# Performance work log

Hardware: AMD Instinct MI355X
Metric: run time of the kernel (lower is better)

The kernel has to match this reference:

```python
import jax, jax.numpy as jnp
import numpy as np


def setup_inputs() -> dict:
    key = jax.random.key(0)
    k1, k2 = jax.random.split(key)
    N, D = 8192, 64
    mag = jax.random.uniform(k1, (N, D), dtype=jnp.float32)
    phase = jax.random.normal(k2, (N, D), dtype=jnp.float32)
    return {"mag": mag, "phase": phase}


def reference(mag, phase):
    # score_ij = sum_d mag_i,d * mag_j,d * cos(phase_i,d - phase_j,d)
    # expanded via cos(a-b) = cos a cos b + sin a sin b into two GEMMs,
    # mathematically identical to the O(N^2 D) broadcasted form.
    a = mag * jnp.cos(phase)  # [N, D]
    b = mag * jnp.sin(phase)  # [N, D]
    scores = a @ a.T + b @ b.T  # [N, N]
    attn = jax.nn.softmax(scores, axis=1)
    new_mag = attn @ mag      # [N, D]
    new_phase = attn @ phase  # [N, D]
    return new_mag, new_phase
```

## Files before the change

kernel.cpp:

```cpp
#include <hip/hip_runtime.h>
#include <hip/hip_bf16.h>

typedef __attribute__((ext_vector_type(8))) short short8;
typedef __attribute__((ext_vector_type(4))) float f32x4;
typedef __attribute__((ext_vector_type(16))) float f32x16;
typedef __attribute__((ext_vector_type(2))) int int2v;

#define N_TOK 8192
#define D_HALF 64
#define D_FULL 128
#define QB 64
#define KHALF 4096
#define CHUNK 128
#define NCH (KHALF / CHUNK)
#define OSTR 132
#define THR 8.0f

__global__ __launch_bounds__(256) void precompute_kernel(
    const float* __restrict__ mag, const float* __restrict__ phase,
    __hip_bfloat16* __restrict__ Kf, __hip_bfloat16* __restrict__ Vf)
{
    int idx = blockIdx.x * 256 + threadIdx.x;
    if (idx >= N_TOK * D_HALF) return;
    int n = idx >> 6, d0 = idx & 63;
    float m = mag[idx], p = phase[idx];
    float s, c;
    sincosf(p, &s, &c);
    {
        float val[2] = { m * c, m * s };
        #pragma unroll
        for (int h = 0; h < 2; ++h) {
            int dc = d0 + 64 * h;
            int off = ((n >> 5) * 16 + (dc >> 4) * 2 + ((dc >> 3) & 1)) * 256
                      + (n & 31) * 8 + (dc & 7);
            Kf[off] = __float2bfloat16(val[h]);
        }
    }
    {
        float val[2] = { m, p };
        #pragma unroll
        for (int h = 0; h < 2; ++h) {
            int dv = d0 + 64 * h;
            int off = ((n >> 4) * 4 + (dv >> 5)) * 512 + ((n >> 3) & 1) * 256
                      + (dv & 31) * 8 + (n & 7);
            Vf[off] = __float2bfloat16(val[h]);
        }
    }
}

static __device__ __forceinline__ unsigned bfpair(float lo, float hi)
{
    __hip_bfloat16 l = __float2bfloat16(lo), h = __float2bfloat16(hi);
    unsigned short ul = *reinterpret_cast<unsigned short*>(&l);
    unsigned short uh = *reinterpret_cast<unsigned short*>(&h);
    return (unsigned)ul | ((unsigned)uh << 16);
}

__global__ __launch_bounds__(512, 2) void attn_kernel(
    const short8* __restrict__ Kf8, const short8* __restrict__ Vf8,
    float* __restrict__ Opart, float* __restrict__ Mp, float* __restrict__ Sp)
{
    __shared__ __align__(16) char smem[68608];
    short8* ldsK = (short8*)smem;
    short8* ldsV = (short8*)(smem + 32768);
    float (*O_lds)[32][OSTR] = (float (*)[32][OSTR])smem;
    float* ms_base = (float*)(smem + 67584);

    const int tid  = threadIdx.x;
    const int wid  = tid >> 6;
    const int lane = tid & 63;
    const int li   = lane & 31;
    const int hi   = lane >> 5;
    const int qh   = wid >> 2;
    const int kp   = wid & 3;

    const int bid  = blockIdx.x;
    const int qt   = bid >> 1;
    const int kh   = bid & 1;
    const int rot  = bid & 31;

    auto msm = [&](int slot, int which) -> float* { return ms_base + (slot * 2 + which) * 32; };

    auto stage = [&](const short8* gsrc, char* lbase) {
        const char* g = (const char*)gsrc;
        #pragma unroll
        for (int j = 0; j < 4; ++j)
            __builtin_amdgcn_global_load_lds(
                (const __attribute__((address_space(1))) void*)(g + j * 8192 + tid * 16),
                (__attribute__((address_space(3))) void*)(lbase + j * 8192 + wid * 1024),
                16, 0, 0);
    };

    short8 bq[8];
    {
        const short8* qp = Kf8 + (size_t)(qt * 2 + qh) * 512;
        #pragma unroll
        for (int ks = 0; ks < 8; ++ks)
            bq[ks] = qp[(ks * 2 + hi) * 32 + li];
    }

    f32x16 acc[4];
    #pragma unroll
    for (int d = 0; d < 4; ++d) acc[d] = (f32x16)(0.0f);
    float mrow = -3.0e38f, srow = 0.0f;

    {
        int ck0 = kh * NCH + rot;
        stage(Kf8 + (size_t)ck0 * 2048, smem);
        stage(Vf8 + (size_t)ck0 * 2048, smem + 32768);
    }
    __syncthreads();

    for (int t = 0; t < NCH; ++t) {
        f32x16 st = (f32x16)(0.0f);
        __builtin_amdgcn_s_setprio(1);
        #pragma unroll
        for (int ks = 0; ks < 8; ++ks) {
            short8 kf = ldsK[kp * 512 + (ks * 2 + hi) * 32 + li];
            st = __builtin_amdgcn_mfma_f32_32x32x16_bf16(kf, bq[ks], st, 0, 0, 0);
        }
        __builtin_amdgcn_s_setprio(0);

        float mx[8];
        #pragma unroll
        for (int r = 0; r < 8; ++r) mx[r] = fmaxf(st[r], st[r + 8]);
        #pragma unroll
        for (int w = 4; w >= 1; w >>= 1)
            #pragma unroll
            for (int r = 0; r < w; ++r) mx[r] = fmaxf(mx[r], mx[r + w]);
        float pmax = fmaxf(mx[0], __shfl_xor(mx[0], 32));

        if (!__all(pmax - mrow <= THR)) {
            float mn  = fmaxf(mrow, pmax);
            float scl = __expf(mrow - mn);
            srow *= scl;
            #pragma unroll
            for (int d = 0; d < 4; ++d)
                #pragma unroll
                for (int r = 0; r < 16; ++r) acc[d][r] *= scl;
            mrow = mn;
        }

        #pragma unroll
        for (int r = 0; r < 16; ++r) st[r] = __expf(st[r] - mrow);
        float sm[8];
        #pragma unroll
        for (int r = 0; r < 8; ++r) sm[r] = st[r] + st[r + 8];
        #pragma unroll
        for (int w = 4; w >= 1; w >>= 1)
            #pragma unroll
            for (int r = 0; r < w; ++r) sm[r] += sm[r + w];
        srow += sm[0] + __shfl_xor(sm[0], 32);

        __syncthreads();
        if (t + 1 < NCH) {
            int ck = kh * NCH + ((t + 1 + rot) & (NCH - 1));
            stage(Kf8 + (size_t)ck * 2048, smem);
        }

        #pragma unroll
        for (int c = 0; c < 2; ++c) {
            const int b = 8 * c;
            unsigned a0 = bfpair(st[b + 0], st[b + 1]);
            unsigned a1 = bfpair(st[b + 2], st[b + 3]);
            unsigned b0 = bfpair(st[b + 4], st[b + 5]);
            unsigned b1 = bfpair(st[b + 6], st[b + 7]);
            int2v r0 = __builtin_amdgcn_permlane32_swap((int)a0, (int)b0, false, false);
            int2v r1 = __builtin_amdgcn_permlane32_swap((int)a1, (int)b1, false, false);
            union { int w[4]; short8 v; } u;
            u.w[0] = r0[0]; u.w[1] = r1[0]; u.w[2] = r0[1]; u.w[3] = r1[1];

            const short8* vp = ldsV + (kp * 2 + c) * 256 + hi * 32 + li;
            __builtin_amdgcn_s_setprio(1);
            #pragma unroll
            for (int d = 0; d < 4; ++d) {
                short8 vf = vp[d * 64];
                acc[d] = __builtin_amdgcn_mfma_f32_32x32x16_bf16(vf, u.v, acc[d], 0, 0, 0);
            }
            __builtin_amdgcn_s_setprio(0);
        }

        __syncthreads();
        if (t + 1 < NCH) {
            int ck = kh * NCH + ((t + 1 + rot) & (NCH - 1));
            stage(Vf8 + (size_t)ck * 2048, smem + 32768);
        }
    }

    auto store_partial = [&](int slot) {
        #pragma unroll
        for (int d = 0; d < 4; ++d)
            #pragma unroll
            for (int rr = 0; rr < 4; ++rr) {
                f32x4 v;
                #pragma unroll
                for (int j = 0; j < 4; ++j) v[j] = acc[d][4 * rr + j];
                *reinterpret_cast<f32x4*>(&O_lds[slot][li][d * 32 + 8 * rr + 4 * hi]) = v;
            }
        if (hi == 0) { msm(slot, 0)[li] = mrow; msm(slot, 1)[li] = srow; }
    };
    auto merge_partial = [&](int slot) {
        float mb = msm(slot, 0)[li], sb = msm(slot, 1)[li];
        float M  = fmaxf(mrow, mb);
        float ea = __expf(mrow - M), eb = __expf(mb - M);
        srow = srow * ea + sb * eb;
        mrow = M;
        #pragma unroll
        for (int d = 0; d < 4; ++d)
            #pragma unroll
            for (int rr = 0; rr < 4; ++rr) {
                f32x4 v = *reinterpret_cast<const f32x4*>(&O_lds[slot][li][d * 32 + 8 * rr + 4 * hi]);
                #pragma unroll
                for (int j = 0; j < 4; ++j)
                    acc[d][4 * rr + j] = acc[d][4 * rr + j] * ea + v[j] * eb;
            }
    };

    __syncthreads();
    if (kp >= 2) store_partial(qh * 2 + (kp - 2));
    __syncthreads();
    if (kp < 2) merge_partial(qh * 2 + kp);
    __syncthreads();
    if (kp < 2) store_partial(qh * 2 + kp);
    __syncthreads();

    #pragma unroll
    for (int u0 = 0; u0 < 2; ++u0) {
        int u  = tid + u0 * 512;
        int q  = u >> 4;
        int dg = (u & 15) * 8;
        int grp = q >> 5, qq = q & 31;
        float m0 = msm(grp * 2 + 0, 0)[qq], s0 = msm(grp * 2 + 0, 1)[qq];
        float m1 = msm(grp * 2 + 1, 0)[qq], s1 = msm(grp * 2 + 1, 1)[qq];
        float M  = fmaxf(m0, m1);
        float e0 = __expf(m0 - M), e1 = __expf(m1 - M);
        float S  = s0 * e0 + s1 * e1;
        f32x4 o0, o1;
        #pragma unroll
        for (int j = 0; j < 4; ++j) {
            o0[j] = O_lds[grp * 2 + 0][qq][dg + j]     * e0 + O_lds[grp * 2 + 1][qq][dg + j]     * e1;
            o1[j] = O_lds[grp * 2 + 0][qq][dg + 4 + j] * e0 + O_lds[grp * 2 + 1][qq][dg + 4 + j] * e1;
        }
        size_t pidx = (size_t)bid * QB + q;
        *reinterpret_cast<f32x4*>(&Opart[pidx * D_FULL + dg])     = o0;
        *reinterpret_cast<f32x4*>(&Opart[pidx * D_FULL + dg + 4]) = o1;
        if (dg == 0) { Mp[pidx] = M; Sp[pidx] = S; }
    }
}

__global__ __launch_bounds__(256) void merge2_kernel(
    const float* __restrict__ Opart, const float* __restrict__ Mp,
    const float* __restrict__ Sp, float* __restrict__ out)
{
    int i   = blockIdx.x * 256 + threadIdx.x;
    int row = i >> 5;
    int dg  = (i & 31) * 4;
    int qt  = row >> 6, qq = row & 63;
    size_t p0 = (size_t)(qt * 2 + 0) * QB + qq;
    size_t p1 = (size_t)(qt * 2 + 1) * QB + qq;
    float m0 = Mp[p0], m1 = Mp[p1], s0 = Sp[p0], s1 = Sp[p1];
    float M  = fmaxf(m0, m1);
    float e0 = __expf(m0 - M), e1 = __expf(m1 - M);
    float inv = 1.0f / (s0 * e0 + s1 * e1);
    f32x4 a = *reinterpret_cast<const f32x4*>(&Opart[p0 * D_FULL + dg]);
    f32x4 b = *reinterpret_cast<const f32x4*>(&Opart[p1 * D_FULL + dg]);
    f32x4 o;
    #pragma unroll
    for (int j = 0; j < 4; ++j) o[j] = (a[j] * e0 + b[j] * e1) * inv;
    float* dst = (dg < D_HALF)
        ? out + (size_t)row * D_HALF + dg
        : out + (size_t)N_TOK * D_HALF + (size_t)row * D_HALF + (dg - D_HALF);
    *reinterpret_cast<f32x4*>(dst) = o;
}

extern "C" void kernel_launch(void* const* d_in, const int* in_sizes, int n_in,
                              void* d_out, int out_size, void* d_ws, size_t ws_size,
                              hipStream_t stream)
{
    const float* mag   = (const float*)d_in[0];
    const float* phase = (const float*)d_in[1];
    float* out = (float*)d_out;

    char* ws = (char*)d_ws;
    __hip_bfloat16* Kf = (__hip_bfloat16*)ws;
    __hip_bfloat16* Vf = Kf + (size_t)N_TOK * D_FULL;
    float* Opart = (float*)(ws + 4u * 1024 * 1024);
    float* Mp    = (float*)(ws + 12u * 1024 * 1024);
    float* Sp    = Mp + 16384;

    precompute_kernel<<<(N_TOK * D_HALF + 255) / 256, 256, 0, stream>>>(mag, phase, Kf, Vf);
    attn_kernel<<<256, 512, 0, stream>>>((const short8*)Kf, (const short8*)Vf, Opart, Mp, Sp);
    merge2_kernel<<<1024, 256, 0, stream>>>(Opart, Mp, Sp, out);
}
```

Before: 66.31 us.

## Widen query tile to 128, split keys four ways, double-buffer K/V staging

Each block now covers 128 query rows against a quarter of the keys. Eight waves form four query groups of two key-panel waves, so each staged K/V chunk feeds twice as many queries. K and V are staged together into two 64KB LDS buffers, with the chunk two steps ahead prefetched through global_load_lds and waited on with explicit vmcnt. This replaces the per-iteration split K/V restaging and its extra syncthreads. In exchange, LDS use grows to 128KB, which likely caps occupancy at one block per CU. The final merge also reads four partials per row instead of two, doubling partial-output traffic.

```diff
diff --git a/kernel.cpp b/kernel.cpp
--- a/kernel.cpp
+++ b/kernel.cpp
@@ -9,10 +9,10 @@
 #define N_TOK 8192
 #define D_HALF 64
 #define D_FULL 128
-#define QB 64
-#define KHALF 4096
+#define QB 128
+#define KQ 2048
 #define CHUNK 128
-#define NCH (KHALF / CHUNK)
+#define NCH (KQ / CHUNK)
 #define OSTR 132
 #define THR 8.0f
 
@@ -60,40 +60,46 @@
     const short8* __restrict__ Kf8, const short8* __restrict__ Vf8,
     float* __restrict__ Opart, float* __restrict__ Mp, float* __restrict__ Sp)
 {
-    __shared__ __align__(16) char smem[68608];
-    short8* ldsK = (short8*)smem;
-    short8* ldsV = (short8*)(smem + 32768);
-    float (*O_lds)[32][OSTR] = (float (*)[32][OSTR])smem;
-    float* ms_base = (float*)(smem + 67584);
+    __shared__ __align__(16) char smem[131072];
 
     const int tid  = threadIdx.x;
     const int wid  = tid >> 6;
     const int lane = tid & 63;
     const int li   = lane & 31;
     const int hi   = lane >> 5;
-    const int qh   = wid >> 2;
-    const int kp   = wid & 3;
+    const int qh   = wid >> 1;
+    const int kp   = wid & 1;
 
     const int bid  = blockIdx.x;
-    const int qt   = bid >> 1;
-    const int kh   = bid & 1;
-    const int rot  = bid & 31;
-
+    const int qt   = bid >> 2;
+    const int kq   = bid & 3;
+    const int rot  = bid & (NCH - 1);
+
+    float (*O_lds)[32][OSTR] = (float (*)[32][OSTR])smem;
+    float* ms_base = (float*)(smem + 67584);
     auto msm = [&](int slot, int which) -> float* { return ms_base + (slot * 2 + which) * 32; };
 
-    auto stage = [&](const short8* gsrc, char* lbase) {
-        const char* g = (const char*)gsrc;
+    auto stageKV = [&](int ck, char* lbase) {
+        const char* gk = (const char*)(Kf8 + (size_t)ck * 2048);
+        const char* gv = (const char*)(Vf8 + (size_t)ck * 2048);
         #pragma unroll
         for (int j = 0; j < 4; ++j)
             __builtin_amdgcn_global_load_lds(
-                (const __attribute__((address_space(1))) void*)(g + j * 8192 + tid * 16),
-                (__attribute__((address_space(3))) void*)(lbase + j * 8192 + wid * 1024),
+                (const __attribute__((address_space(1))) void*)(gk + j * 8192 + tid * 16),
+                (__attribute__((address_space(3))) void*)(lbase + j * 8192 + tid * 16),
+                16, 0, 0);
+        #pragma unroll
+        for (int j = 0; j < 4; ++j)
+            __builtin_amdgcn_global_load_lds(
+                (const __attribute__((address_space(1))) void*)(gv + j * 8192 + tid * 16),
+                (__attribute__((address_space(3))) void*)(lbase + 32768 + j * 8192 + tid * 16),
                 16, 0, 0);
     };
+    auto ck_of = [&](int t) { return kq * NCH + ((t + rot) & (NCH - 1)); };
 
     short8 bq[8];
     {
-        const short8* qp = Kf8 + (size_t)(qt * 2 + qh) * 512;
+        const short8* qp = Kf8 + (size_t)(qt * 4 + qh) * 512;
         #pragma unroll
         for (int ks = 0; ks < 8; ++ks)
             bq[ks] = qp[(ks * 2 + hi) * 32 + li];
@@ -104,87 +110,91 @@
     for (int d = 0; d < 4; ++d) acc[d] = (f32x16)(0.0f);
     float mrow = -3.0e38f, srow = 0.0f;
 
-    {
-        int ck0 = kh * NCH + rot;
-        stage(Kf8 + (size_t)ck0 * 2048, smem);
-        stage(Vf8 + (size_t)ck0 * 2048, smem + 32768);
-    }
-    __syncthreads();
+    stageKV(ck_of(0), smem);
+    stageKV(ck_of(1), smem + 65536);
+    asm volatile("s_waitcnt vmcnt(8)");
+    __builtin_amdgcn_s_barrier();
 
     for (int t = 0; t < NCH; ++t) {
-        f32x16 st = (f32x16)(0.0f);
-        __builtin_amdgcn_s_setprio(1);
-        #pragma unroll
-        for (int ks = 0; ks < 8; ++ks) {
-            short8 kf = ldsK[kp * 512 + (ks * 2 + hi) * 32 + li];
-            st = __builtin_amdgcn_mfma_f32_32x32x16_bf16(kf, bq[ks], st, 0, 0, 0);
+        char* base = smem + (t & 1) * 65536;
+        const short8* ldsK = (const short8*)base;
+        const short8* ldsV = (const short8*)(base + 32768);
+
+        #pragma unroll
+        for (int pp = 0; pp < 2; ++pp) {
+            const int panel = kp + 2 * pp;
+
+            f32x16 st = (f32x16)(0.0f);
+            __builtin_amdgcn_s_setprio(1);
+            #pragma unroll
+            for (int ks = 0; ks < 8; ++ks) {
+                short8 kf = ldsK[panel * 512 + (ks * 2 + hi) * 32 + li];
+                st = __builtin_amdgcn_mfma_f32_32x32x16_bf16(kf, bq[ks], st, 0, 0, 0);
+            }
+            __builtin_amdgcn_s_setprio(0);
+
+            float mx[8];
+            #pragma unroll
+            for (int r = 0; r < 8; ++r) mx[r] = fmaxf(st[r], st[r + 8]);
+            #pragma unroll
+            for (int w = 4; w >= 1; w >>= 1)
+                #pragma unroll
+                for (int r = 0; r < w; ++r) mx[r] = fmaxf(mx[r], mx[r + w]);
+            float pmax = fmaxf(mx[0], __shfl_xor(mx[0], 32));
+
+            if (!__all(pmax - mrow <= THR)) {
+                float mn  = fmaxf(mrow, pmax);
+                float scl = __expf(mrow - mn);
+                srow *= scl;
+                #pragma unroll
+                for (int d = 0; d < 4; ++d)
+                    #pragma unroll
+                    for (int r = 0; r < 16; ++r) acc[d][r] *= scl;
+                mrow = mn;
+            }
+
+            #pragma unroll
+            for (int r = 0; r < 16; ++r) st[r] = __expf(st[r] - mrow);
+            float sm[8];
+            #pragma unroll
+            for (int r = 0; r < 8; ++r) sm[r] = st[r] + st[r + 8];
+            #pragma unroll
+            for (int w = 4; w >= 1; w >>= 1)
+                #pragma unroll
+                for (int r = 0; r < w; ++r) sm[r] += sm[r + w];
+            srow += sm[0] + __shfl_xor(sm[0], 32);
+
+            #pragma unroll
+            for (int c = 0; c < 2; ++c) {
+                const int b = 8 * c;
+                unsigned a0 = bfpair(st[b + 0], st[b + 1]);
+                unsigned a1 = bfpair(st[b + 2], st[b + 3]);
+                unsigned b0 = bfpair(st[b + 4], st[b + 5]);
+                unsigned b1 = bfpair(st[b + 6], st[b + 7]);
+                int2v r0 = __builtin_amdgcn_permlane32_swap((int)a0, (int)b0, false, false);
+                int2v r1 = __builtin_amdgcn_permlane32_swap((int)a1, (int)b1, false, false);
+                union { int w[4]; short8 v; } u;
+                u.w[0] = r0[0]; u.w[1] = r1[0]; u.w[2] = r0[1]; u.w[3] = r1[1];
+
+                const short8* vp = ldsV + (panel * 2 + c) * 256 + hi * 32 + li;
+                __builtin_amdgcn_s_setprio(1);
+                #pragma unroll
+                for (int d = 0; d < 4; ++d) {
+                    short8 vf = vp[d * 64];
+                    acc[d] = __builtin_amdgcn_mfma_f32_32x32x16_bf16(vf, u.v, acc[d], 0, 0, 0);
+                }
+                __builtin_amdgcn_s_setprio(0);
+            }
         }
-        __builtin_amdgcn_s_setprio(0);
-
-        float mx[8];
-        #pragma unroll
-        for (int r = 0; r < 8; ++r) mx[r] = fmaxf(st[r], st[r + 8]);
-        #pragma unroll
-        for (int w = 4; w >= 1; w >>= 1)
-            #pragma unroll
-            for (int r = 0; r < w; ++r) mx[r] = fmaxf(mx[r], mx[r + w]);
-        float pmax = fmaxf(mx[0], __shfl_xor(mx[0], 32));
-
-        if (!__all(pmax - mrow <= THR)) {
-            float mn  = fmaxf(mrow, pmax);
-            float scl = __expf(mrow - mn);
-            srow *= scl;
-            #pragma unroll
-            for (int d = 0; d < 4; ++d)
-                #pragma unroll
-                for (int r = 0; r < 16; ++r) acc[d][r] *= scl;
-            mrow = mn;
+
+        __builtin_amdgcn_s_barrier();
+        if (t + 2 < NCH) {
+            stageKV(ck_of(t + 2), base);
+            asm volatile("s_waitcnt vmcnt(8)");
+        } else {
+            asm volatile("s_waitcnt vmcnt(0)");
         }
-
-        #pragma unroll
-        for (int r = 0; r < 16; ++r) st[r] = __expf(st[r] - mrow);
-        float sm[8];
-        #pragma unroll
-        for (int r = 0; r < 8; ++r) sm[r] = st[r] + st[r + 8];
-        #pragma unroll
-        for (int w = 4; w >= 1; w >>= 1)
-            #pragma unroll
-            for (int r = 0; r < w; ++r) sm[r] += sm[r + w];
-        srow += sm[0] + __shfl_xor(sm[0], 32);
-
-        __syncthreads();
-        if (t + 1 < NCH) {
-            int ck = kh * NCH + ((t + 1 + rot) & (NCH - 1));
-            stage(Kf8 + (size_t)ck * 2048, smem);
-        }
-
-        #pragma unroll
-        for (int c = 0; c < 2; ++c) {
-            const int b = 8 * c;
-            unsigned a0 = bfpair(st[b + 0], st[b + 1]);
-            unsigned a1 = bfpair(st[b + 2], st[b + 3]);
-            unsigned b0 = bfpair(st[b + 4], st[b + 5]);
-            unsigned b1 = bfpair(st[b + 6], st[b + 7]);
-            int2v r0 = __builtin_amdgcn_permlane32_swap((int)a0, (int)b0, false, false);
-            int2v r1 = __builtin_amdgcn_permlane32_swap((int)a1, (int)b1, false, false);
-            union { int w[4]; short8 v; } u;
-            u.w[0] = r0[0]; u.w[1] = r1[0]; u.w[2] = r0[1]; u.w[3] = r1[1];
-
-            const short8* vp = ldsV + (kp * 2 + c) * 256 + hi * 32 + li;
-            __builtin_amdgcn_s_setprio(1);
-            #pragma unroll
-            for (int d = 0; d < 4; ++d) {
-                short8 vf = vp[d * 64];
-                acc[d] = __builtin_amdgcn_mfma_f32_32x32x16_bf16(vf, u.v, acc[d], 0, 0, 0);
-            }
-            __builtin_amdgcn_s_setprio(0);
-        }
-
-        __syncthreads();
-        if (t + 1 < NCH) {
-            int ck = kh * NCH + ((t + 1 + rot) & (NCH - 1));
-            stage(Vf8 + (size_t)ck * 2048, smem + 32768);
-        }
+        __builtin_amdgcn_s_barrier();
     }
 
     auto store_partial = [&](int slot) {
@@ -217,56 +227,58 @@
     };
 
     __syncthreads();
-    if (kp >= 2) store_partial(qh * 2 + (kp - 2));
+    if (kp == 1) store_partial(qh);
     __syncthreads();
-    if (kp < 2) merge_partial(qh * 2 + kp);
+    if (kp == 0) merge_partial(qh);
     __syncthreads();
-    if (kp < 2) store_partial(qh * 2 + kp);
+    if (kp == 0) store_partial(qh);
     __syncthreads();
 
     #pragma unroll
-    for (int u0 = 0; u0 < 2; ++u0) {
+    for (int u0 = 0; u0 < 4; ++u0) {
         int u  = tid + u0 * 512;
         int q  = u >> 4;
         int dg = (u & 15) * 8;
         int grp = q >> 5, qq = q & 31;
-        float m0 = msm(grp * 2 + 0, 0)[qq], s0 = msm(grp * 2 + 0, 1)[qq];
-        float m1 = msm(grp * 2 + 1, 0)[qq], s1 = msm(grp * 2 + 1, 1)[qq];
-        float M  = fmaxf(m0, m1);
-        float e0 = __expf(m0 - M), e1 = __expf(m1 - M);
-        float S  = s0 * e0 + s1 * e1;
-        f32x4 o0, o1;
-        #pragma unroll
-        for (int j = 0; j < 4; ++j) {
-            o0[j] = O_lds[grp * 2 + 0][qq][dg + j]     * e0 + O_lds[grp * 2 + 1][qq][dg + j]     * e1;
-            o1[j] = O_lds[grp * 2 + 0][qq][dg + 4 + j] * e0 + O_lds[grp * 2 + 1][qq][dg + 4 + j] * e1;
-        }
+        f32x4 o0 = *reinterpret_cast<const f32x4*>(&O_lds[grp][qq][dg]);
+        f32x4 o1 = *reinterpret_cast<const f32x4*>(&O_lds[grp][qq][dg + 4]);
         size_t pidx = (size_t)bid * QB + q;
         *reinterpret_cast<f32x4*>(&Opart[pidx * D_FULL + dg])     = o0;
         *reinterpret_cast<f32x4*>(&Opart[pidx * D_FULL + dg + 4]) = o1;
-        if (dg == 0) { Mp[pidx] = M; Sp[pidx] = S; }
-    }
-}
-
-__global__ __launch_bounds__(256) void merge2_kernel(
+        if (dg == 0) { Mp[pidx] = msm(grp, 0)[qq]; Sp[pidx] = msm(grp, 1)[qq]; }
+    }
+}
+
+__global__ __launch_bounds__(256) void merge4_kernel(
     const float* __restrict__ Opart, const float* __restrict__ Mp,
     const float* __restrict__ Sp, float* __restrict__ out)
 {
     int i   = blockIdx.x * 256 + threadIdx.x;
     int row = i >> 5;
     int dg  = (i & 31) * 4;
-    int qt  = row >> 6, qq = row & 63;
-    size_t p0 = (size_t)(qt * 2 + 0) * QB + qq;
-    size_t p1 = (size_t)(qt * 2 + 1) * QB + qq;
-    float m0 = Mp[p0], m1 = Mp[p1], s0 = Sp[p0], s1 = Sp[p1];
-    float M  = fmaxf(m0, m1);
-    float e0 = __expf(m0 - M), e1 = __expf(m1 - M);
-    float inv = 1.0f / (s0 * e0 + s1 * e1);
-    f32x4 a = *reinterpret_cast<const f32x4*>(&Opart[p0 * D_FULL + dg]);
-    f32x4 b = *reinterpret_cast<const f32x4*>(&Opart[p1 * D_FULL + dg]);
-    f32x4 o;
-    #pragma unroll
-    for (int j = 0; j < 4; ++j) o[j] = (a[j] * e0 + b[j] * e1) * inv;
+    int qt  = row >> 7, qq = row & 127;
+    size_t pidx[4];
+    float m[4], s[4];
+    #pragma unroll
+    for (int k = 0; k < 4; ++k) {
+        pidx[k] = (size_t)(qt * 4 + k) * QB + qq;
+        m[k] = Mp[pidx[k]];
+        s[k] = Sp[pidx[k]];
+    }
+    float M = fmaxf(fmaxf(m[0], m[1]), fmaxf(m[2], m[3]));
+    float e[4], S = 0.0f;
+    #pragma unroll
+    for (int k = 0; k < 4; ++k) { e[k] = __expf(m[k] - M); S += s[k] * e[k]; }
+    float inv = 1.0f / S;
+    f32x4 o = (f32x4)(0.0f);
+    #pragma unroll
+    for (int k = 0; k < 4; ++k) {
+        f32x4 a = *reinterpret_cast<const f32x4*>(&Opart[pidx[k] * D_FULL + dg]);
+        #pragma unroll
+        for (int j = 0; j < 4; ++j) o[j] += a[j] * e[k];
+    }
+    #pragma unroll
+    for (int j = 0; j < 4; ++j) o[j] *= inv;
     float* dst = (dg < D_HALF)
         ? out + (size_t)row * D_HALF + dg
         : out + (size_t)N_TOK * D_HALF + (size_t)row * D_HALF + (dg - D_HALF);
@@ -285,10 +297,10 @@
     __hip_bfloat16* Kf = (__hip_bfloat16*)ws;
     __hip_bfloat16* Vf = Kf + (size_t)N_TOK * D_FULL;
     float* Opart = (float*)(ws + 4u * 1024 * 1024);
-    float* Mp    = (float*)(ws + 12u * 1024 * 1024);
-    float* Sp    = Mp + 16384;
+    float* Mp    = (float*)(ws + 20u * 1024 * 1024);
+    float* Sp    = Mp + 32768;
 
     precompute_kernel<<<(N_TOK * D_HALF + 255) / 256, 256, 0, stream>>>(mag, phase, Kf, Vf);
     attn_kernel<<<256, 512, 0, stream>>>((const short8*)Kf, (const short8*)Vf, Opart, Mp, Sp);
-    merge2_kernel<<<1024, 256, 0, stream>>>(Opart, Mp, Sp, out);
-}
+    merge4_kernel<<<1024, 256, 0, stream>>>(Opart, Mp, Sp, out);
+}
```

New measurement: 64.92 us. 1.02x faster.
